# Kernel optimization log

Hardware: AMD Instinct MI355X
Metric: run time of the kernel (lower is better)

The kernel has to match this reference:

```python
import jax, jax.numpy as jnp
import numpy as np

B, N, D, H = 4, 1024, 1024, 16
Dh = D // H


def setup_inputs() -> dict:
    key = jax.random.key(0)
    ks = jax.random.split(key, 5)
    w = 0.02
    return {
        "x": jax.random.normal(ks[0], (B, N, D), dtype=jnp.float32),
        "Wq": jax.random.normal(ks[1], (D, D), dtype=jnp.float32) * w,
        "bq": jnp.zeros((D,), dtype=jnp.float32),
        "Wk": jax.random.normal(ks[2], (D, D), dtype=jnp.float32) * w,
        "bk": jnp.zeros((D,), dtype=jnp.float32),
        "Wv": jax.random.normal(ks[3], (D, D), dtype=jnp.float32) * w,
        "bv": jnp.zeros((D,), dtype=jnp.float32),
        "Wc": jax.random.normal(ks[4], (D, D), dtype=jnp.float32) * w,
        "bc": jnp.zeros((D,), dtype=jnp.float32),
    }


def reference(x, Wq, bq, Wk, bk, Wv, bv, Wc, bc):
    # q/k/v projections: nn.Linear computes x @ W.T + b
    q = jnp.einsum("bnd,ed->bne", x, Wq) + bq
    k = jnp.einsum("bnd,ed->bne", x, Wk) + bk
    v = jnp.einsum("bnd,ed->bne", x, Wv) + bv
    # split heads: [B,N,D] -> [B,H,N,Dh]
    qh = q.reshape(B, N, H, Dh).transpose(0, 2, 1, 3)
    kh = k.reshape(B, N, H, Dh).transpose(0, 2, 1, 3)
    vh = v.reshape(B, N, H, Dh).transpose(0, 2, 1, 3)
    # NOTE (faithful quirk): original uses scale = q.size(1) = seq_len N,
    # not head_dim, so scores are scaled by N**-0.5.
    scale = jnp.float32(N) ** -0.5
    scores = jnp.einsum("bhnd,bhmd->bhnm", qh, kh) * scale  # [B,H,N,N]
    attn = jax.nn.softmax(scores, axis=-1)
    # attn_dropout = 0.0 -> identity
    o = jnp.einsum("bhnm,bhmd->bhnd", attn, vh)  # [B,H,N,Dh]
    # NOTE (faithful quirk): original does v.resize(original_size) on the
    # contiguous [B,H,N,Dh] tensor, reinterpreting memory as [B,N,D]
    # WITHOUT permuting heads back. Replicate exactly:
    o = o.reshape(B, N, D)
    out = jnp.einsum("bnd,ed->bne", o, Wc) + bc
    return out
```

## Files before the change

kernel.cpp:

```cpp
#include <hip/hip_runtime.h>
#include <cstddef>
#include <cstdint>

#define B_  4
#define N_  1024
#define D_  1024
#define H_  16
#define DH  64
#define M_  4096

#define SC2 0.04508422f

typedef __attribute__((ext_vector_type(4))) float   f32x4;
typedef __attribute__((ext_vector_type(8))) __bf16  bf16x8;

#define MFMA(a, b, c) __builtin_amdgcn_mfma_f32_16x16x32_bf16((a), (b), (c), 0, 0, 0)
#define GLDS(gp, lp) __builtin_amdgcn_global_load_lds( \
    (__attribute__((address_space(1))) void*)(gp),     \
    (__attribute__((address_space(3))) void*)(lp), 16, 0, 0)

__global__ __launch_bounds__(256) void convert_k(
    const float* __restrict__ x,  const float* __restrict__ Wq,
    const float* __restrict__ Wk, const float* __restrict__ Wv,
    const float* __restrict__ Wc,
    __bf16* __restrict__ xb, __bf16* __restrict__ wqkvb,
    __bf16* __restrict__ wcb)
{
    const unsigned u = blockIdx.x * 256u + threadIdx.x;
    const unsigned e = u * 8u;
    const float* src;
    __bf16* dst;
    if (e < 4194304u) { src = x + e; dst = xb + e; }
    else {
        const unsigned t2 = e - 4194304u;
        const unsigned wsel = t2 >> 20;
        const unsigned wo = t2 & 1048575u;
        src = (wsel == 0 ? Wq : wsel == 1 ? Wk : wsel == 2 ? Wv : Wc) + wo;
        dst = (wsel < 3 ? wqkvb + (size_t)wsel * 1048576u : wcb) + wo;
    }
    const float4 f0 = *(const float4*)(src);
    const float4 f1 = *(const float4*)(src + 4);
    bf16x8 r;
    r[0] = (__bf16)f0.x; r[1] = (__bf16)f0.y; r[2] = (__bf16)f0.z; r[3] = (__bf16)f0.w;
    r[4] = (__bf16)f1.x; r[5] = (__bf16)f1.y; r[6] = (__bf16)f1.z; r[7] = (__bf16)f1.w;
    *(bf16x8*)dst = r;
}

__global__ __launch_bounds__(512, 2) void gemm_qkv256(
    const __bf16* __restrict__ xb, const __bf16* __restrict__ Wb,
    const float* __restrict__ bq, const float* __restrict__ bk,
    const float* __restrict__ bv,
    __bf16* __restrict__ qk_out, __bf16* __restrict__ vT)
{
    __shared__ __bf16 ring[65536];

    const int tid  = threadIdx.x;
    const int w    = tid >> 6;
    const int lane = tid & 63;
    const int quad = lane >> 4;
    const int l15  = lane & 15;
    const int wr   = w >> 2;
    const int wc   = w & 3;

    const int bid = blockIdx.x;
    const bool VT = (bid >= 128);
    int m0, n0;
    const __bf16 *Ap, *Bp;
    if (!VT) { m0 = (bid >> 3) * 256; n0 = (bid & 7) * 256; Ap = xb; Bp = Wb; }
    else {
        const int v = bid - 128;
        m0 = (v & 3) * 256;
        n0 = (v >> 2) * 256;
        Ap = Wb + (size_t)2 * D_ * D_; Bp = xb;
    }

    const size_t sgl = (size_t)(w * 16 + l15) * D_ + quad * 8;
    const __bf16* Asrc = Ap + (size_t)m0 * D_ + sgl;
    const __bf16* Bsrc = Bp + (size_t)n0 * D_ + sgl;
    __bf16* const ringA = ring;
    __bf16* const ringB = ring + 32768;
    const int sdst = w * 1024;

#define STG_A(tt, h) do {                                               \
    const __bf16* s_ = Asrc + (size_t)(h) * 128 * D_ + (tt) * 64;       \
    __bf16* d_ = ringA + ((((tt) & 1) * 2 + (h)) * 8192) + sdst;        \
    GLDS(s_, d_); GLDS(s_ + 32, d_ + 512); } while (0)
#define STG_B(tt, h) do {                                               \
    const __bf16* s_ = Bsrc + (size_t)(h) * 128 * D_ + (tt) * 64;       \
    __bf16* d_ = ringB + ((((tt) & 1) * 2 + (h)) * 8192) + sdst;        \
    GLDS(s_, d_); GLDS(s_ + 32, d_ + 512); } while (0)

    f32x4 acc[8][4];
    #pragma unroll
    for (int i = 0; i < 8; ++i)
        #pragma unroll
        for (int j = 0; j < 4; ++j)
            acc[i][j] = (f32x4){0.f, 0.f, 0.f, 0.f};

    STG_B(0, 0); STG_B(0, 1);
    STG_A(0, 0); STG_A(0, 1);
    STG_B(1, 0); STG_B(1, 1);

    const int rdo = lane * 8;

#define READ_A(q)                                                       \
    afr[0][0] = *(const bf16x8*)(Asl + ((2*(q)  )*2 + 0)*512);          \
    afr[0][1] = *(const bf16x8*)(Asl + ((2*(q)  )*2 + 1)*512);          \
    afr[1][0] = *(const bf16x8*)(Asl + ((2*(q)+1)*2 + 0)*512);          \
    afr[1][1] = *(const bf16x8*)(Asl + ((2*(q)+1)*2 + 1)*512);

#define PHASE_MFMA(q)                                                   \
    __builtin_amdgcn_s_barrier();                                       \
    asm volatile("s_waitcnt lgkmcnt(0)" ::: "memory");                  \
    __builtin_amdgcn_s_setprio(1);                                      \
    _Pragma("unroll")                                                   \
    for (int i = 0; i < 2; ++i)                                         \
      _Pragma("unroll")                                                 \
      for (int nt = 0; nt < 4; ++nt) {                                  \
        acc[2*(q)+i][nt] = MFMA(afr[i][0], bfr[nt][0], acc[2*(q)+i][nt]); \
        acc[2*(q)+i][nt] = MFMA(afr[i][1], bfr[nt][1], acc[2*(q)+i][nt]); \
      }                                                                 \
    __builtin_amdgcn_s_setprio(0);

    for (int t = 0; t < 16; ++t) {
        if (t < 15) asm volatile("s_waitcnt vmcnt(4)" ::: "memory");
        else        asm volatile("s_waitcnt vmcnt(0)" ::: "memory");
        __builtin_amdgcn_s_barrier();

        const __bf16* Asl = ringA + ((t & 1) * 2 + wr) * 8192 + rdo;
        const __bf16* Bsl = ringB + ((t & 1) * 2 + (wc >> 1)) * 8192
                                  + (wc & 1) * 4096 + rdo;
        bf16x8 afr[2][2], bfr[4][2];

        if (t < 15) STG_A(t + 1, 0);
        #pragma unroll
        for (int nt = 0; nt < 4; ++nt) {
            bfr[nt][0] = *(const bf16x8*)(Bsl + (nt * 2 + 0) * 512);
            bfr[nt][1] = *(const bf16x8*)(Bsl + (nt * 2 + 1) * 512);
        }
        READ_A(0)
        PHASE_MFMA(0)
        __builtin_amdgcn_s_barrier();

        if (t < 15) STG_A(t + 1, 1);
        READ_A(1)
        PHASE_MFMA(1)
        __builtin_amdgcn_s_barrier();

        if (t < 14) STG_B(t + 2, 0);
        READ_A(2)
        PHASE_MFMA(2)
        __builtin_amdgcn_s_barrier();

        if (t < 14) STG_B(t + 2, 1);
        READ_A(3)
        PHASE_MFMA(3)
    }
#undef STG_A
#undef STG_B
#undef READ_A
#undef PHASE_MFMA

    if (!VT) {
        const int zq = n0 >> 10;
        const float* bias = zq ? bk : bq;
        const float qs = zq ? 1.0f : SC2;
        const int nb = (n0 & 1023) + wc * 64;
        float bvv[4];
        #pragma unroll
        for (int nt = 0; nt < 4; ++nt) bvv[nt] = bias[nb + nt * 16 + l15];
        __bf16* C = qk_out + (size_t)zq * M_ * D_;
        #pragma unroll
        for (int mt = 0; mt < 8; ++mt) {
            #pragma unroll
            for (int r = 0; r < 4; ++r) {
                const int row = m0 + wr * 128 + mt * 16 + quad * 4 + r;
                #pragma unroll
                for (int nt = 0; nt < 4; ++nt) {
                    const int col = nb + nt * 16 + l15;
                    const size_t idx = (((size_t)(row >> 10) * H_ + (col >> 6)) * N_
                                        + (row & 1023)) * DH + (col & 63);
                    C[idx] = (__bf16)((acc[mt][nt][r] + bvv[nt]) * qs);
                }
            }
        }
    } else {
        #pragma unroll
        for (int mt = 0; mt < 8; ++mt) {
            #pragma unroll
            for (int r = 0; r < 4; ++r) {
                const int row = m0 + wr * 128 + mt * 16 + quad * 4 + r;
                const float brow = bv[row];
                #pragma unroll
                for (int nt = 0; nt < 4; ++nt) {
                    const int col = n0 + wc * 64 + nt * 16 + l15;
                    const size_t idx = (((size_t)(col >> 10) * H_ + (row >> 6)) * DH
                                        + (row & 63)) * N_ + (col & 1023);
                    vT[idx] = (__bf16)(acc[mt][nt][r] + brow);
                }
            }
        }
    }
}

__global__ __launch_bounds__(256, 6) void gemm_out(
    const __bf16* __restrict__ A0, const __bf16* __restrict__ Wb,
    const float* __restrict__ b0, float* __restrict__ Cb)
{
    __shared__ __bf16 As[2048];
    __shared__ __bf16 Bs[4096];

    const int tid  = threadIdx.x;
    const int w    = tid >> 6;
    const int lane = tid & 63;
    const int quad = lane >> 4;
    const int l15  = lane & 15;
    const int wr   = w >> 1, wc = w & 1;

    const int m0 = blockIdx.y * 64;
    const int n0 = blockIdx.x * 128;

    const int Tt = tid >> 6, ko = (tid >> 4) & 3, l = tid & 15;
    const size_t aoff  = (size_t)(m0 + Tt * 16 + l) * D_ + ko * 8;
    const size_t boff1 = (size_t)(n0 + Tt * 16 + l) * D_ + ko * 8;
    const size_t boff2 = boff1 + (size_t)64 * D_;
    __bf16* adst  = As + w * 512;
    __bf16* bdst1 = Bs + w * 512;
    __bf16* bdst2 = Bs + 2048 + w * 512;

    f32x4 acc[2][4];
    #pragma unroll
    for (int i = 0; i < 2; ++i)
        #pragma unroll
        for (int j = 0; j < 4; ++j)
            acc[i][j] = (f32x4){0.f, 0.f, 0.f, 0.f};

    for (int k0 = 0; k0 < D_; k0 += 32) {
        GLDS(A0 + aoff  + k0, adst);
        GLDS(Wb + boff1 + k0, bdst1);
        GLDS(Wb + boff2 + k0, bdst2);
        __syncthreads();

        bf16x8 af[2], bf[4];
        #pragma unroll
        for (int mt = 0; mt < 2; ++mt)
            af[mt] = *(const bf16x8*)(As + (((wr * 2 + mt) * 4 + quad) * 16 + l15) * 8);
        #pragma unroll
        for (int nt = 0; nt < 4; ++nt)
            bf[nt] = *(const bf16x8*)(Bs + (((wc * 4 + nt) * 4 + quad) * 16 + l15) * 8);
        #pragma unroll
        for (int mt = 0; mt < 2; ++mt)
            #pragma unroll
            for (int nt = 0; nt < 4; ++nt)
                acc[mt][nt] = MFMA(af[mt], bf[nt], acc[mt][nt]);
        __syncthreads();
    }

    float bvv[4];
    #pragma unroll
    for (int nt = 0; nt < 4; ++nt)
        bvv[nt] = b0[n0 + wc * 64 + nt * 16 + l15];
    #pragma unroll
    for (int mt = 0; mt < 2; ++mt) {
        #pragma unroll
        for (int r = 0; r < 4; ++r) {
            const int row = m0 + (wr * 2 + mt) * 16 + quad * 4 + r;
            #pragma unroll
            for (int nt = 0; nt < 4; ++nt) {
                const int col = n0 + wc * 64 + nt * 16 + l15;
                Cb[(size_t)row * D_ + col] = acc[mt][nt][r] + bvv[nt];
            }
        }
    }
}

#define SP  68

__global__ __launch_bounds__(256, 3) void attn_mfma(
    const __bf16* __restrict__ qh, const __bf16* __restrict__ kh,
    const __bf16* __restrict__ vT, __bf16* __restrict__ ob)
{
    __shared__ __bf16 Ks[2 * 4096];
    __shared__ __bf16 Vs[2 * 4096];
    __shared__ float  Ps[4][16 * SP];

    const int tid  = threadIdx.x;
    const int w    = tid >> 6;
    const int lane = tid & 63;
    const int quad = lane >> 4;
    const int l15  = lane & 15;

    const int bh = blockIdx.x & 63;
    const int qt = blockIdx.x >> 6;
    const int b  = bh >> 4;
    const int h  = bh & 15;

    const __bf16* qp = qh + ((size_t)(b * H_ + h) * N_ + qt * 64 + w * 16 + l15) * DH + quad * 8;
    const bf16x8 qf0 = *(const bf16x8*)(qp);
    const bf16x8 qf1 = *(const bf16x8*)(qp + 32);

    const int c1 = tid, c2 = tid + 256;
    const int nt1 = c1 >> 7, ko1 = (c1 >> 4) & 7, l1 = c1 & 15;
    const int nt2 = c2 >> 7, ko2 = (c2 >> 4) & 7, l2 = c2 & 15;
    const __bf16* khead = kh + (size_t)(b * H_ + h) * N_ * DH;
    const __bf16* vhead = vT + (size_t)(b * H_ + h) * DH * N_;
    const size_t koff1 = (size_t)(nt1 * 16 + l1) * DH + ko1 * 8;
    const size_t koff2 = (size_t)(nt2 * 16 + l2) * DH + ko2 * 8;
    const size_t voff1 = (size_t)(nt1 * 16 + l1) * N_ + ko1 * 8;
    const size_t voff2 = (size_t)(nt2 * 16 + l2) * N_ + ko2 * 8;

#define STG_KV(kt, p) do {                                              \
    const size_t kb_ = (size_t)(kt) * 64;                               \
    GLDS(khead + kb_ * DH + koff1, Ks + (p) * 4096 + w * 512);          \
    GLDS(khead + kb_ * DH + koff2, Ks + (p) * 4096 + 2048 + w * 512);   \
    GLDS(vhead + kb_ + voff1,      Vs + (p) * 4096 + w * 512);          \
    GLDS(vhead + kb_ + voff2,      Vs + (p) * 4096 + 2048 + w * 512);   \
} while (0)

    float psum[4] = {0.f, 0.f, 0.f, 0.f};
    f32x4 Ov[4];
    #pragma unroll
    for (int nt = 0; nt < 4; ++nt) Ov[nt] = (f32x4){0.f, 0.f, 0.f, 0.f};

    STG_KV(0, 0);

    for (int kt = 0; kt < 16; ++kt) {
        asm volatile("s_waitcnt vmcnt(0)" ::: "memory");
        __builtin_amdgcn_s_barrier();
        asm volatile("" ::: "memory");

        if (kt < 15) STG_KV(kt + 1, (kt + 1) & 1);

        const __bf16* Kb = Ks + (kt & 1) * 4096;
        const __bf16* Vb = Vs + (kt & 1) * 4096;

        f32x4 sa[4];
        __builtin_amdgcn_s_setprio(1);
        #pragma unroll
        for (int nt = 0; nt < 4; ++nt) {
            const bf16x8 kf0 = *(const bf16x8*)(Kb + (nt * 128 + quad * 16 + l15) * 8);
            const bf16x8 kf1 = *(const bf16x8*)(Kb + (nt * 128 + (quad + 4) * 16 + l15) * 8);
            sa[nt] = (f32x4){0.f, 0.f, 0.f, 0.f};
            sa[nt] = MFMA(qf0, kf0, sa[nt]);
            sa[nt] = MFMA(qf1, kf1, sa[nt]);
        }
        __builtin_amdgcn_s_setprio(0);

        #pragma unroll
        for (int nt = 0; nt < 4; ++nt) {
            #pragma unroll
            for (int r = 0; r < 4; ++r) {
                const float p = __builtin_exp2f(sa[nt][r]);
                psum[r] += p;
                Ps[w][(quad * 4 + r) * SP + nt * 16 + l15] = p;
            }
        }

        __builtin_amdgcn_s_setprio(1);
        #pragma unroll
        for (int kw = 0; kw < 2; ++kw) {
            const f32x4 pa = *(const f32x4*)&Ps[w][l15 * SP + kw * 32 + quad * 8];
            const f32x4 pb = *(const f32x4*)&Ps[w][l15 * SP + kw * 32 + quad * 8 + 4];
            bf16x8 pf;
            #pragma unroll
            for (int j = 0; j < 4; ++j) { pf[j] = (__bf16)pa[j]; pf[4 + j] = (__bf16)pb[j]; }
            #pragma unroll
            for (int nt = 0; nt < 4; ++nt) {
                const bf16x8 vf = *(const bf16x8*)(Vb + (nt * 128 + (kw * 4 + quad) * 16 + l15) * 8);
                Ov[nt] = MFMA(pf, vf, Ov[nt]);
            }
        }
        __builtin_amdgcn_s_setprio(0);
    }
#undef STG_KV

    float lrow[4];
    #pragma unroll
    for (int r = 0; r < 4; ++r) {
        float lt = psum[r];
        lt += __shfl_xor(lt, 1);
        lt += __shfl_xor(lt, 2);
        lt += __shfl_xor(lt, 4);
        lt += __shfl_xor(lt, 8);
        lrow[r] = lt;
    }

    #pragma unroll
    for (int r = 0; r < 4; ++r) {
        const float inv = 1.0f / lrow[r];
        const int row = qt * 64 + w * 16 + quad * 4 + r;
        __bf16* op = ob + ((size_t)(b * H_ + h) * N_ + row) * DH + l15;
        #pragma unroll
        for (int nt = 0; nt < 4; ++nt)
            op[nt * 16] = (__bf16)(Ov[nt][r] * inv);
    }
}

extern "C" void kernel_launch(void* const* d_in, const int* in_sizes, int n_in,
                              void* d_out, int out_size, void* d_ws, size_t ws_size,
                              hipStream_t stream) {
    const float* x  = (const float*)d_in[0];
    const float* Wq = (const float*)d_in[1];
    const float* bq = (const float*)d_in[2];
    const float* Wk = (const float*)d_in[3];
    const float* bk = (const float*)d_in[4];
    const float* Wv = (const float*)d_in[5];
    const float* bv = (const float*)d_in[6];
    const float* Wc = (const float*)d_in[7];
    const float* bc = (const float*)d_in[8];
    float* out = (float*)d_out;

    char* base = (char*)d_ws;
    __bf16* xb    = (__bf16*)(base);
    __bf16* wqkvb = (__bf16*)(base + (size_t)8  * 1048576);
    __bf16* wcb   = (__bf16*)(base + (size_t)14 * 1048576);
    __bf16* qkvb  = (__bf16*)(base + (size_t)16 * 1048576);
    __bf16* vTb   = (__bf16*)(base + (size_t)40 * 1048576);
    __bf16* obf   = (__bf16*)(base);

    __bf16* qhb = qkvb;
    __bf16* khb = qkvb + (size_t)M_ * D_;

    convert_k<<<dim3(4096), dim3(256), 0, stream>>>(
        x, Wq, Wk, Wv, Wc, xb, wqkvb, wcb);

    gemm_qkv256<<<dim3(192), dim3(512), 0, stream>>>(
        xb, wqkvb, bq, bk, bv, qkvb, vTb);

    attn_mfma<<<dim3(1024), dim3(256), 0, stream>>>(qhb, khb, vTb, obf);

    gemm_out<<<dim3(8, 64, 1), dim3(256), 0, stream>>>(obf, wcb, bc, out);
}
```

Baseline: 204.8 us.

## Rewrite attention with 32x32 MFMA, register-resident P, and register-staged K/V

The attention kernel now has each wave own 32 query rows and uses 32x32x16 bf16 MFMAs, computing S transposed so that the exponentiated probabilities stay in registers. They are packed into bf16 operands with cvt_pk and permlane32_swap instead of making a round trip through LDS. K/V tiles are prefetched into registers and written to a single LDS buffer, with two barriers per iteration, replacing the double-buffered global_load_lds scheme. Each block now covers 128 query rows, so the grid halves and occupancy is declared as 2 blocks per CU. The added barriers and single buffering may expose load latency.

```diff
diff --git a/kernel.cpp b/kernel.cpp
--- a/kernel.cpp
+++ b/kernel.cpp
@@ -11,13 +11,22 @@
 
 #define SC2 0.04508422f
 
-typedef __attribute__((ext_vector_type(4))) float   f32x4;
-typedef __attribute__((ext_vector_type(8))) __bf16  bf16x8;
-
-#define MFMA(a, b, c) __builtin_amdgcn_mfma_f32_16x16x32_bf16((a), (b), (c), 0, 0, 0)
+typedef __attribute__((ext_vector_type(4)))  float   f32x4;
+typedef __attribute__((ext_vector_type(16))) float   f32x16;
+typedef __attribute__((ext_vector_type(8)))  __bf16  bf16x8;
+typedef __attribute__((ext_vector_type(4)))  unsigned int u32x4;
+
+#define MFMA(a, b, c)   __builtin_amdgcn_mfma_f32_16x16x32_bf16((a), (b), (c), 0, 0, 0)
+#define MFMA32(a, b, c) __builtin_amdgcn_mfma_f32_32x32x16_bf16((a), (b), (c), 0, 0, 0)
 #define GLDS(gp, lp) __builtin_amdgcn_global_load_lds( \
     (__attribute__((address_space(1))) void*)(gp),     \
     (__attribute__((address_space(3))) void*)(lp), 16, 0, 0)
+
+static __device__ __forceinline__ unsigned cvtpk(float lo, float hi) {
+    unsigned r;
+    asm("v_cvt_pk_bf16_f32 %0, %1, %2" : "=v"(r) : "v"(lo), "v"(hi));
+    return r;
+}
 
 __global__ __launch_bounds__(256) void convert_k(
     const float* __restrict__ x,  const float* __restrict__ Wq,
@@ -274,125 +283,144 @@
     }
 }
 
-#define SP  68
-
-__global__ __launch_bounds__(256, 3) void attn_mfma(
+__global__ __launch_bounds__(256, 2) void attn_mfma(
     const __bf16* __restrict__ qh, const __bf16* __restrict__ kh,
     const __bf16* __restrict__ vT, __bf16* __restrict__ ob)
 {
-    __shared__ __bf16 Ks[2 * 4096];
-    __shared__ __bf16 Vs[2 * 4096];
-    __shared__ float  Ps[4][16 * SP];
+    __shared__ __align__(16) __bf16 Ks[4096];
+    __shared__ __align__(16) __bf16 Vs[4096];
 
     const int tid  = threadIdx.x;
     const int w    = tid >> 6;
     const int lane = tid & 63;
-    const int quad = lane >> 4;
-    const int l15  = lane & 15;
-
-    const int bh = blockIdx.x & 63;
-    const int qt = blockIdx.x >> 6;
+    const int la31 = lane & 31;
+    const int hi   = lane >> 5;
+
+    const int bh = blockIdx.x >> 3;
+    const int qt = blockIdx.x & 7;
     const int b  = bh >> 4;
     const int h  = bh & 15;
 
-    const __bf16* qp = qh + ((size_t)(b * H_ + h) * N_ + qt * 64 + w * 16 + l15) * DH + quad * 8;
+    const size_t headQ = (size_t)(b * H_ + h) * N_;
+
+    const int qrow = qt * 128 + w * 32 + la31;
+    const __bf16* qp = qh + (headQ + qrow) * DH + hi * 8;
     const bf16x8 qf0 = *(const bf16x8*)(qp);
-    const bf16x8 qf1 = *(const bf16x8*)(qp + 32);
-
-    const int c1 = tid, c2 = tid + 256;
-    const int nt1 = c1 >> 7, ko1 = (c1 >> 4) & 7, l1 = c1 & 15;
-    const int nt2 = c2 >> 7, ko2 = (c2 >> 4) & 7, l2 = c2 & 15;
-    const __bf16* khead = kh + (size_t)(b * H_ + h) * N_ * DH;
+    const bf16x8 qf1 = *(const bf16x8*)(qp + 16);
+    const bf16x8 qf2 = *(const bf16x8*)(qp + 32);
+    const bf16x8 qf3 = *(const bf16x8*)(qp + 48);
+
+    const __bf16* khead = kh + headQ * DH;
     const __bf16* vhead = vT + (size_t)(b * H_ + h) * DH * N_;
-    const size_t koff1 = (size_t)(nt1 * 16 + l1) * DH + ko1 * 8;
-    const size_t koff2 = (size_t)(nt2 * 16 + l2) * DH + ko2 * 8;
-    const size_t voff1 = (size_t)(nt1 * 16 + l1) * N_ + ko1 * 8;
-    const size_t voff2 = (size_t)(nt2 * 16 + l2) * N_ + ko2 * 8;
-
-#define STG_KV(kt, p) do {                                              \
-    const size_t kb_ = (size_t)(kt) * 64;                               \
-    GLDS(khead + kb_ * DH + koff1, Ks + (p) * 4096 + w * 512);          \
-    GLDS(khead + kb_ * DH + koff2, Ks + (p) * 4096 + 2048 + w * 512);   \
-    GLDS(vhead + kb_ + voff1,      Vs + (p) * 4096 + w * 512);          \
-    GLDS(vhead + kb_ + voff2,      Vs + (p) * 4096 + 2048 + w * 512);   \
+
+    const size_t koff0 = (size_t)la31 * DH + w * 16 + hi * 8;
+    const size_t koff1 = koff0 + (size_t)32 * DH;
+    const size_t voff0 = (size_t)((w & 1) * 32 + la31) * N_ + (w >> 1) * 16 + hi * 8;
+    const size_t voff1 = voff0 + 32;
+    __bf16* const kd0 = Ks + tid * 8;
+    __bf16* const kd1 = Ks + tid * 8 + 2048;
+    __bf16* const vd0 = Vs + tid * 8;
+    __bf16* const vd1 = Vs + tid * 8 + 2048;
+
+    f32x16 Ov0, Ov1;
+    #pragma unroll
+    for (int r = 0; r < 16; ++r) { Ov0[r] = 0.f; Ov1[r] = 0.f; }
+    float psum = 0.f;
+
+    bf16x8 kr0 = *(const bf16x8*)(khead + koff0);
+    bf16x8 kr1 = *(const bf16x8*)(khead + koff1);
+    bf16x8 vr0 = *(const bf16x8*)(vhead + voff0);
+    bf16x8 vr1 = *(const bf16x8*)(vhead + voff1);
+
+#define PACK(earr, base, dst) do {                                        \
+    unsigned U_ = cvtpk(earr[(base) + 0], earr[(base) + 1]);              \
+    unsigned W_ = cvtpk(earr[(base) + 2], earr[(base) + 3]);              \
+    unsigned V_ = cvtpk(earr[(base) + 4], earr[(base) + 5]);              \
+    unsigned Z_ = cvtpk(earr[(base) + 6], earr[(base) + 7]);              \
+    asm volatile("v_permlane32_swap_b32 %0, %1" : "+v"(U_), "+v"(V_));    \
+    asm volatile("v_permlane32_swap_b32 %0, %1" : "+v"(W_), "+v"(Z_));    \
+    u32x4 pw_ = {U_, W_, V_, Z_};                                         \
+    dst = __builtin_bit_cast(bf16x8, pw_);                                \
 } while (0)
 
-    float psum[4] = {0.f, 0.f, 0.f, 0.f};
-    f32x4 Ov[4];
-    #pragma unroll
-    for (int nt = 0; nt < 4; ++nt) Ov[nt] = (f32x4){0.f, 0.f, 0.f, 0.f};
-
-    STG_KV(0, 0);
-
     for (int kt = 0; kt < 16; ++kt) {
-        asm volatile("s_waitcnt vmcnt(0)" ::: "memory");
-        __builtin_amdgcn_s_barrier();
-        asm volatile("" ::: "memory");
-
-        if (kt < 15) STG_KV(kt + 1, (kt + 1) & 1);
-
-        const __bf16* Kb = Ks + (kt & 1) * 4096;
-        const __bf16* Vb = Vs + (kt & 1) * 4096;
-
-        f32x4 sa[4];
+        asm volatile("s_waitcnt lgkmcnt(0)" ::: "memory");
+        __builtin_amdgcn_s_barrier();
+        __builtin_amdgcn_sched_barrier(0);
+
+        *(bf16x8*)kd0 = kr0;
+        *(bf16x8*)kd1 = kr1;
+        *(bf16x8*)vd0 = vr0;
+        *(bf16x8*)vd1 = vr1;
+        if (kt < 15) {
+            const __bf16* kp = khead + (size_t)(kt + 1) * 64 * DH;
+            const __bf16* vp = vhead + (size_t)(kt + 1) * 64;
+            kr0 = *(const bf16x8*)(kp + koff0);
+            kr1 = *(const bf16x8*)(kp + koff1);
+            vr0 = *(const bf16x8*)(vp + voff0);
+            vr1 = *(const bf16x8*)(vp + voff1);
+        }
+        asm volatile("s_waitcnt lgkmcnt(0)" ::: "memory");
+        __builtin_amdgcn_s_barrier();
+        __builtin_amdgcn_sched_barrier(0);
+
+        f32x16 sa0, sa1;
         __builtin_amdgcn_s_setprio(1);
-        #pragma unroll
-        for (int nt = 0; nt < 4; ++nt) {
-            const bf16x8 kf0 = *(const bf16x8*)(Kb + (nt * 128 + quad * 16 + l15) * 8);
-            const bf16x8 kf1 = *(const bf16x8*)(Kb + (nt * 128 + (quad + 4) * 16 + l15) * 8);
-            sa[nt] = (f32x4){0.f, 0.f, 0.f, 0.f};
-            sa[nt] = MFMA(qf0, kf0, sa[nt]);
-            sa[nt] = MFMA(qf1, kf1, sa[nt]);
+        {
+            f32x16 z;
+            #pragma unroll
+            for (int r = 0; r < 16; ++r) z[r] = 0.f;
+            bf16x8 kf;
+            kf = *(const bf16x8*)(Ks + 0 * 512 + lane * 8); sa0 = MFMA32(kf, qf0, z);
+            kf = *(const bf16x8*)(Ks + 1 * 512 + lane * 8); sa0 = MFMA32(kf, qf1, sa0);
+            kf = *(const bf16x8*)(Ks + 2 * 512 + lane * 8); sa0 = MFMA32(kf, qf2, sa0);
+            kf = *(const bf16x8*)(Ks + 3 * 512 + lane * 8); sa0 = MFMA32(kf, qf3, sa0);
+            kf = *(const bf16x8*)(Ks + 4 * 512 + lane * 8); sa1 = MFMA32(kf, qf0, z);
+            kf = *(const bf16x8*)(Ks + 5 * 512 + lane * 8); sa1 = MFMA32(kf, qf1, sa1);
+            kf = *(const bf16x8*)(Ks + 6 * 512 + lane * 8); sa1 = MFMA32(kf, qf2, sa1);
+            kf = *(const bf16x8*)(Ks + 7 * 512 + lane * 8); sa1 = MFMA32(kf, qf3, sa1);
         }
         __builtin_amdgcn_s_setprio(0);
 
-        #pragma unroll
-        for (int nt = 0; nt < 4; ++nt) {
-            #pragma unroll
-            for (int r = 0; r < 4; ++r) {
-                const float p = __builtin_exp2f(sa[nt][r]);
-                psum[r] += p;
-                Ps[w][(quad * 4 + r) * SP + nt * 16 + l15] = p;
-            }
-        }
+        float e0[16], e1[16];
+        #pragma unroll
+        for (int r = 0; r < 16; ++r) { e0[r] = __builtin_exp2f(sa0[r]); psum += e0[r]; }
+        #pragma unroll
+        for (int r = 0; r < 16; ++r) { e1[r] = __builtin_exp2f(sa1[r]); psum += e1[r]; }
+
+        bf16x8 pf0, pf1, pf2, pf3;
+        PACK(e0, 0, pf0);
+        PACK(e0, 8, pf1);
+        PACK(e1, 0, pf2);
+        PACK(e1, 8, pf3);
 
         __builtin_amdgcn_s_setprio(1);
-        #pragma unroll
-        for (int kw = 0; kw < 2; ++kw) {
-            const f32x4 pa = *(const f32x4*)&Ps[w][l15 * SP + kw * 32 + quad * 8];
-            const f32x4 pb = *(const f32x4*)&Ps[w][l15 * SP + kw * 32 + quad * 8 + 4];
-            bf16x8 pf;
-            #pragma unroll
-            for (int j = 0; j < 4; ++j) { pf[j] = (__bf16)pa[j]; pf[4 + j] = (__bf16)pb[j]; }
-            #pragma unroll
-            for (int nt = 0; nt < 4; ++nt) {
-                const bf16x8 vf = *(const bf16x8*)(Vb + (nt * 128 + (kw * 4 + quad) * 16 + l15) * 8);
-                Ov[nt] = MFMA(pf, vf, Ov[nt]);
-            }
+        {
+            bf16x8 vf;
+            vf = *(const bf16x8*)(Vs + 0 * 512 + lane * 8); Ov0 = MFMA32(pf0, vf, Ov0);
+            vf = *(const bf16x8*)(Vs + 2 * 512 + lane * 8); Ov0 = MFMA32(pf1, vf, Ov0);
+            vf = *(const bf16x8*)(Vs + 4 * 512 + lane * 8); Ov0 = MFMA32(pf2, vf, Ov0);
+            vf = *(const bf16x8*)(Vs + 6 * 512 + lane * 8); Ov0 = MFMA32(pf3, vf, Ov0);
+            vf = *(const bf16x8*)(Vs + 1 * 512 + lane * 8); Ov1 = MFMA32(pf0, vf, Ov1);
+            vf = *(const bf16x8*)(Vs + 3 * 512 + lane * 8); Ov1 = MFMA32(pf1, vf, Ov1);
+            vf = *(const bf16x8*)(Vs + 5 * 512 + lane * 8); Ov1 = MFMA32(pf2, vf, Ov1);
+            vf = *(const bf16x8*)(Vs + 7 * 512 + lane * 8); Ov1 = MFMA32(pf3, vf, Ov1);
         }
         __builtin_amdgcn_s_setprio(0);
     }
-#undef STG_KV
-
-    float lrow[4];
-    #pragma unroll
-    for (int r = 0; r < 4; ++r) {
-        float lt = psum[r];
-        lt += __shfl_xor(lt, 1);
-        lt += __shfl_xor(lt, 2);
-        lt += __shfl_xor(lt, 4);
-        lt += __shfl_xor(lt, 8);
-        lrow[r] = lt;
-    }
-
-    #pragma unroll
-    for (int r = 0; r < 4; ++r) {
-        const float inv = 1.0f / lrow[r];
-        const int row = qt * 64 + w * 16 + quad * 4 + r;
-        __bf16* op = ob + ((size_t)(b * H_ + h) * N_ + row) * DH + l15;
-        #pragma unroll
-        for (int nt = 0; nt < 4; ++nt)
-            op[nt * 16] = (__bf16)(Ov[nt][r] * inv);
+#undef PACK
+
+    psum += __shfl_xor(psum, 32);
+    const float inv = 1.0f / psum;
+
+    __bf16* const obase = ob + (headQ + qt * 128 + w * 32) * DH;
+    #pragma unroll
+    for (int r = 0; r < 16; ++r) {
+        const int q_r = (r & 3) + 8 * (r >> 2) + 4 * hi;
+        const float ivr = __shfl(inv, q_r);
+        __bf16* op = obase + (size_t)q_r * DH + la31;
+        op[0]  = (__bf16)(Ov0[r] * ivr);
+        op[32] = (__bf16)(Ov1[r] * ivr);
     }
 }
 
@@ -427,7 +455,7 @@
     gemm_qkv256<<<dim3(192), dim3(512), 0, stream>>>(
         xb, wqkvb, bq, bk, bv, qkvb, vTb);
 
-    attn_mfma<<<dim3(1024), dim3(256), 0, stream>>>(qhb, khb, vTb, obf);
+    attn_mfma<<<dim3(512), dim3(256), 0, stream>>>(qhb, khb, vTb, obf);
 
     gemm_out<<<dim3(8, 64, 1), dim3(256), 0, stream>>>(obf, wcb, bc, out);
 }
```

After: 184.1 us. 10.1% less time.
